# Optimization experiments

Measured on AMD Instinct MI355X. Metric: run time of the kernel, lower is better.

## Reference

```python
import jax, jax.numpy as jnp
import numpy as np

B, L, D, H = 4, 2048, 1024, 16
DH = D // H
SCALE = DH ** -0.5


def setup_inputs() -> dict:
    key = jax.random.key(0)
    ks = jax.random.split(key, 8)
    q = jax.random.normal(ks[0], (B, L, D), dtype=jnp.float32)
    k = jax.random.normal(ks[1], (B, L, D), dtype=jnp.float32)
    v = jax.random.normal(ks[2], (B, L, D), dtype=jnp.float32)
    mask = jax.random.randint(ks[3], (B, 1, L), 0, 2, dtype=jnp.int32)
    s = D ** -0.5
    Wq = jax.random.normal(ks[4], (D, D), dtype=jnp.float32) * s
    Wk = jax.random.normal(ks[5], (D, D), dtype=jnp.float32) * s
    Wv = jax.random.normal(ks[6], (D, D), dtype=jnp.float32) * s
    Wo = jax.random.normal(ks[7], (D, D), dtype=jnp.float32) * s
    return {"q": q, "k": k, "v": v, "mask": mask, "Wq": Wq, "Wk": Wk, "Wv": Wv, "Wo": Wo}


def reference(q, k, v, mask, Wq, Wk, Wv, Wo):
    b, l, d = q.shape
    # torch Linear (no bias): x @ W^T; split heads -> [B, H, T, DH]
    qh = (q @ Wq.T).reshape(b, l, H, DH).transpose(0, 2, 1, 3)
    kh = (k @ Wk.T).reshape(b, -1, H, DH).transpose(0, 2, 1, 3)
    vh = (v @ Wv.T).reshape(b, -1, H, DH).transpose(0, 2, 1, 3)
    # scores [B, H, L, S]
    scores = jnp.einsum('bhld,bhsd->bhls', qh, kh) * SCALE
    scores = jnp.where(mask[:, None, :, :] != 1, jnp.float32(-1e9), scores)
    attn = jax.nn.softmax(scores, axis=-1)  # dropout defined but never applied in original forward
    out = jnp.einsum('bhls,bhsd->bhld', attn, vh)
    out = out.transpose(0, 2, 1, 3).reshape(b, l, d)
    return out @ Wo.T
```

## Files before the change

### kernel.cpp

```cpp
#include <hip/hip_runtime.h>
#include <cstddef>
#include <cstdint>

#define BB 4
#define LL 2048
#define DD 1024
#define HH 16
#define DHD 64
#define QSCALE 0.18033688f

typedef short s16x8 __attribute__((ext_vector_type(8)));
typedef short s16x4 __attribute__((ext_vector_type(4)));
typedef float f32x4 __attribute__((ext_vector_type(4)));
typedef unsigned int u32;
typedef u32 u32x2 __attribute__((ext_vector_type(2)));

__device__ __forceinline__ short f2bf(float f) {
  union { float f; u32 u; } x; x.f = f;
  u32 r = x.u + 0x7FFFu + ((x.u >> 16) & 1u);
  return (short)(r >> 16);
}
__device__ __forceinline__ u32 pack2bf(float a, float b) {
  union { float f; u32 u; } x, y; x.f = a; y.f = b;
  return __builtin_amdgcn_perm(y.u + 0x8000u, x.u + 0x8000u, 0x07060302u);
}
__device__ __forceinline__ void gl2lds16(const short* g, short* l) {
  __builtin_amdgcn_global_load_lds(
      (const __attribute__((address_space(1))) unsigned int*)g,
      (__attribute__((address_space(3))) unsigned int*)l, 16, 0, 0);
}

__global__ __launch_bounds__(256) void cast_x_kernel(const float* __restrict__ q,
                                                     const float* __restrict__ k,
                                                     const float* __restrict__ v,
                                                     short* __restrict__ qb,
                                                     short* __restrict__ kb,
                                                     short* __restrict__ vb) {
  const float* s; short* d;
  if (blockIdx.y == 0) { s = q; d = qb; }
  else if (blockIdx.y == 1) { s = k; d = kb; }
  else { s = v; d = vb; }
  int i = blockIdx.x * 256 + threadIdx.x;
  float4 x = ((const float4*)s)[i];
  s16x4 o; o.x = f2bf(x.x); o.y = f2bf(x.y); o.z = f2bf(x.z); o.w = f2bf(x.w);
  ((s16x4*)d)[i] = o;
}

__global__ __launch_bounds__(256) void cast_w_kernel(const float* __restrict__ Wq,
                                                     const float* __restrict__ Wk,
                                                     const float* __restrict__ Wv,
                                                     const float* __restrict__ Wo,
                                                     short* __restrict__ Wqb,
                                                     short* __restrict__ Wkb,
                                                     short* __restrict__ Wvb,
                                                     short* __restrict__ Wob) {
  const float* s; short* d; float sc = 1.0f;
  if (blockIdx.y == 0) { s = Wq; d = Wqb; sc = QSCALE; }
  else if (blockIdx.y == 1) { s = Wk; d = Wkb; }
  else if (blockIdx.y == 2) { s = Wv; d = Wvb; }
  else { s = Wo; d = Wob; }
  int i = blockIdx.x * 256 + threadIdx.x;
  float4 x = ((const float4*)s)[i];
  s16x4 o; o.x = f2bf(x.x * sc); o.y = f2bf(x.y * sc); o.z = f2bf(x.z * sc); o.w = f2bf(x.w * sc);
  ((s16x4*)d)[i] = o;
}

__global__ __launch_bounds__(256) void mask_kernel(const int* __restrict__ mask,
                                                   float* __restrict__ maskadd) {
  int i = blockIdx.x * 256 + threadIdx.x;
  int4 m = ((const int4*)mask)[i];
  f32x4 o;
  o[0] = (m.x == 1) ? 0.0f : -30000.0f;
  o[1] = (m.y == 1) ? 0.0f : -30000.0f;
  o[2] = (m.z == 1) ? 0.0f : -30000.0f;
  o[3] = (m.w == 1) ? 0.0f : -30000.0f;
  ((f32x4*)maskadd)[i] = o;
}

__device__ __forceinline__ void gemm_core(const short* __restrict__ A, const short* __restrict__ B,
                                          int K, int bm, int bn, short* As, short* Bs,
                                          f32x4 (&acc)[4][4]) {
  const int tid = threadIdx.x;
  const int lane = tid & 63, wave = tid >> 6;
  const int wv = __builtin_amdgcn_readfirstlane(wave);
  const int quad = lane >> 4, l16 = lane & 15;
  const int wm = (wave >> 1) * 64, wn = (wave & 1) * 64;
  const short* ap[4]; const short* bp[4]; short* la[4]; short* lb[4];
#pragma unroll
  for (int t = 0; t < 4; ++t) {
    int s = wv * 256 + t * 64 + lane;
    int r = s >> 3, gl = (s & 7) ^ (r & 7);
    ap[t] = A + (size_t)(bm + r) * K + gl * 8;
    bp[t] = B + (size_t)(bn + r) * K + gl * 8;
    la[t] = &As[(wv * 256 + t * 64) * 8];
    lb[t] = &Bs[(wv * 256 + t * 64) * 8];
  }
  const int sw0 = (quad ^ (l16 & 7)) * 8;
  const int sw1 = ((4 + quad) ^ (l16 & 7)) * 8;
  for (int kk = 0; kk < K; kk += 64) {
    __syncthreads();
#pragma unroll
    for (int t = 0; t < 4; ++t) gl2lds16(ap[t] + kk, la[t]);
#pragma unroll
    for (int t = 0; t < 4; ++t) gl2lds16(bp[t] + kk, lb[t]);
    __syncthreads();
#pragma unroll
    for (int c = 0; c < 2; ++c) {
      const int sw = c ? sw1 : sw0;
      s16x8 af[4], bf[4];
#pragma unroll
      for (int t = 0; t < 4; ++t) af[t] = *(const s16x8*)&As[(wm + t * 16 + l16) * 64 + sw];
#pragma unroll
      for (int t = 0; t < 4; ++t) bf[t] = *(const s16x8*)&Bs[(wn + t * 16 + l16) * 64 + sw];
#pragma unroll
      for (int mt = 0; mt < 4; ++mt)
#pragma unroll
        for (int nt = 0; nt < 4; ++nt)
          acc[mt][nt] = __builtin_amdgcn_mfma_f32_16x16x32_bf16(af[mt], bf[nt], acc[mt][nt], 0, 0, 0);
    }
  }
}

__global__ __launch_bounds__(256) void qkv_gemm(const short* __restrict__ qb, const short* __restrict__ kb,
                                                const short* __restrict__ vb, const short* __restrict__ Wqb,
                                                const short* __restrict__ Wkb, const short* __restrict__ Wvb,
                                                short* __restrict__ Qh, short* __restrict__ Kh,
                                                short* __restrict__ VT) {
  __shared__ short As[128 * 64];
  __shared__ short Bs[128 * 64];
  const int z = blockIdx.z;
  const short *A, *B; short* C;
  if (z == 0) { A = qb; B = Wqb; C = Qh; }
  else if (z == 1) { A = kb; B = Wkb; C = Kh; }
  else { A = Wvb; B = vb; C = VT; }
  const int bm = (z == 2 ? blockIdx.x : (int)blockIdx.y) * 128;
  const int bn = (z == 2 ? (int)blockIdx.y : (int)blockIdx.x) * 128;
  f32x4 acc[4][4] = {};
  gemm_core(A, B, DD, bm, bn, As, Bs, acc);

  const int lane = threadIdx.x & 63, wave = threadIdx.x >> 6;
  const int quad = lane >> 4, l16 = lane & 15;
  const int wm = (wave >> 1) * 64, wn = (wave & 1) * 64;
#pragma unroll
  for (int mt = 0; mt < 4; ++mt)
#pragma unroll
    for (int nt = 0; nt < 4; ++nt)
#pragma unroll
      for (int i = 0; i < 4; ++i) {
        int m = bm + wm + mt * 16 + quad * 4 + i;
        int n = bn + wn + nt * 16 + l16;
        float val = acc[mt][nt][i];
        if (z < 2) {
          int b = m >> 11, l = m & 2047;
          C[((size_t)(b * HH + (n >> 6)) << 17) + (size_t)l * DHD + (n & 63)] = f2bf(val);
        } else {
          int b = n >> 11, l = n & 2047;
          C[((size_t)(b * DD + m) << 11) + l] = f2bf(val);
        }
      }
}

__global__ __launch_bounds__(256) void out_gemm(const short* __restrict__ A, const short* __restrict__ B,
                                                float* __restrict__ C) {
  __shared__ short As[128 * 64];
  __shared__ short Bs[128 * 64];
  const int bm = blockIdx.y * 128, bn = blockIdx.x * 128;
  f32x4 acc[4][4] = {};
  gemm_core(A, B, DD, bm, bn, As, Bs, acc);
  const int lane = threadIdx.x & 63, wave = threadIdx.x >> 6;
  const int quad = lane >> 4, l16 = lane & 15;
  const int wm = (wave >> 1) * 64, wn = (wave & 1) * 64;
#pragma unroll
  for (int mt = 0; mt < 4; ++mt)
#pragma unroll
    for (int nt = 0; nt < 4; ++nt)
#pragma unroll
      for (int i = 0; i < 4; ++i) {
        int m = bm + wm + mt * 16 + quad * 4 + i;
        int n = bn + wn + nt * 16 + l16;
        C[(size_t)m * DD + n] = acc[mt][nt][i];
      }
}

__global__ __launch_bounds__(256, 4) void attn_kernel(const short* __restrict__ Qh,
                                                      const short* __restrict__ Kh,
                                                      const short* __restrict__ VT,
                                                      const float* __restrict__ maskadd,
                                                      short* __restrict__ AO) {
  __shared__ short Ks[64 * 64];
  __shared__ short Vs[64 * 64];
  __shared__ short Pb[8 * 16 * 64];
  const int tid  = threadIdx.x;
  const int lane = tid & 63, wave = tid >> 6;
  const int wv   = __builtin_amdgcn_readfirstlane(wave);
  const int quad = lane >> 4, l16 = lane & 15;
  const int a7 = l16 & 7, q1 = quad >> 1, qlo = quad & 1;
  const int bh = blockIdx.y, b = bh >> 4;
  const int q0 = blockIdx.x * 128;

  const float* mrow = maskadd + b * LL;
  const short* Qb = Qh + (size_t)bh * LL * DHD;
  const short* Kb = Kh + (size_t)bh * LL * DHD;
  const short* Vb = VT + (size_t)bh * DHD * LL;

  s16x8 qf[2][2];
#pragma unroll
  for (int u = 0; u < 2; ++u)
#pragma unroll
    for (int c = 0; c < 2; ++c)
      qf[u][c] = *(const s16x8*)&Qb[(size_t)(q0 + wv * 32 + u * 16 + l16) * DHD + c * 32 + quad * 8];

  const short* kp[2]; const short* vp[2]; short* lk[2]; short* lv[2];
#pragma unroll
  for (int t = 0; t < 2; ++t) {
    int s = wv * 128 + t * 64 + lane;
    int r = s >> 3, gl = (s & 7) ^ (r & 7);
    kp[t] = Kb + (size_t)r * DHD + gl * 8;
    vp[t] = Vb + (size_t)r * LL + gl * 8;
    lk[t] = &Ks[(wv * 128 + t * 64) * 8];
    lv[t] = &Vs[(wv * 128 + t * 64) * 8];
  }
  const int sw0 = (quad ^ a7) * 8;
  const int sw1 = ((4 + quad) ^ a7) * 8;

  s16x8 vone;
#pragma unroll
  for (int j = 0; j < 8; ++j) vone[j] = (short)0x3F80;

  f32x4 lsum[2] = {};
  f32x4 accO[2][4] = {};
  short* pb = &Pb[wave * 2048 + l16 * 64 + qlo * 4];

  for (int s0 = 0; s0 < LL; s0 += 64) {
    f32x4 mm[4];
#pragma unroll
    for (int st = 0; st < 4; ++st) mm[st] = *(const f32x4*)&mrow[s0 + st * 16 + quad * 4];
    __syncthreads();
#pragma unroll
    for (int t = 0; t < 2; ++t) gl2lds16(kp[t] + (size_t)s0 * DHD, lk[t]);
#pragma unroll
    for (int t = 0; t < 2; ++t) gl2lds16(vp[t] + s0, lv[t]);
    __syncthreads();

    s16x8 kf[4][2];
#pragma unroll
    for (int st = 0; st < 4; ++st) {
      kf[st][0] = *(const s16x8*)&Ks[(st * 16 + l16) * 64 + sw0];
      kf[st][1] = *(const s16x8*)&Ks[(st * 16 + l16) * 64 + sw1];
    }
    f32x4 sc[2][4];
#pragma unroll
    for (int u = 0; u < 2; ++u)
#pragma unroll
      for (int st = 0; st < 4; ++st) {
        sc[u][st] = __builtin_amdgcn_mfma_f32_16x16x32_bf16(kf[st][0], qf[u][0], mm[st], 0, 0, 0);
        sc[u][st] = __builtin_amdgcn_mfma_f32_16x16x32_bf16(kf[st][1], qf[u][1], sc[u][st], 0, 0, 0);
      }

#pragma unroll
    for (int u = 0; u < 2; ++u)
#pragma unroll
      for (int st = 0; st < 4; ++st) {
        float p0 = __builtin_amdgcn_exp2f(sc[u][st][0]);
        float p1 = __builtin_amdgcn_exp2f(sc[u][st][1]);
        float p2 = __builtin_amdgcn_exp2f(sc[u][st][2]);
        float p3 = __builtin_amdgcn_exp2f(sc[u][st][3]);
        u32x2 w; w[0] = pack2bf(p0, p1); w[1] = pack2bf(p2, p3);
        *(u32x2*)(pb + u * 1024 + (((st * 2 + q1) ^ a7) << 3)) = w;
      }

    s16x8 pf[2][2];
#pragma unroll
    for (int u = 0; u < 2; ++u)
#pragma unroll
      for (int c = 0; c < 2; ++c)
        pf[u][c] = *(const s16x8*)&Pb[(wave * 2 + u) * 1024 + l16 * 64 + (((c * 4 + quad) ^ a7) << 3)];
#pragma unroll
    for (int u = 0; u < 2; ++u) {
      lsum[u] = __builtin_amdgcn_mfma_f32_16x16x32_bf16(pf[u][0], vone, lsum[u], 0, 0, 0);
      lsum[u] = __builtin_amdgcn_mfma_f32_16x16x32_bf16(pf[u][1], vone, lsum[u], 0, 0, 0);
    }
#pragma unroll
    for (int dt = 0; dt < 4; ++dt) {
      s16x8 vf0 = *(const s16x8*)&Vs[(dt * 16 + l16) * 64 + sw0];
      s16x8 vf1 = *(const s16x8*)&Vs[(dt * 16 + l16) * 64 + sw1];
#pragma unroll
      for (int u = 0; u < 2; ++u) {
        accO[u][dt] = __builtin_amdgcn_mfma_f32_16x16x32_bf16(pf[u][0], vf0, accO[u][dt], 0, 0, 0);
        accO[u][dt] = __builtin_amdgcn_mfma_f32_16x16x32_bf16(pf[u][1], vf1, accO[u][dt], 0, 0, 0);
      }
    }
  }

  short* AOb = AO + (size_t)b * LL * DD + (size_t)(bh & 15) * DHD;
#pragma unroll
  for (int u = 0; u < 2; ++u) {
    f32x4 rl;
#pragma unroll
    for (int i = 0; i < 4; ++i) rl[i] = __builtin_amdgcn_rcpf(lsum[u][i]);
#pragma unroll
    for (int dt = 0; dt < 4; ++dt)
#pragma unroll
      for (int i = 0; i < 4; ++i) {
        int qr = q0 + wv * 32 + u * 16 + quad * 4 + i;
        AOb[(size_t)qr * DD + dt * 16 + l16] = f2bf(accO[u][dt][i] * rl[i]);
      }
  }
}

extern "C" void kernel_launch(void* const* d_in, const int* in_sizes, int n_in,
                              void* d_out, int out_size, void* d_ws, size_t ws_size,
                              hipStream_t stream) {
  const float* q   = (const float*)d_in[0];
  const float* k   = (const float*)d_in[1];
  const float* v   = (const float*)d_in[2];
  const int*  mask = (const int*)d_in[3];
  const float* Wq  = (const float*)d_in[4];
  const float* Wk  = (const float*)d_in[5];
  const float* Wv  = (const float*)d_in[6];
  const float* Wo  = (const float*)d_in[7];

  const size_t SX = (size_t)BB * LL * DD;
  const size_t SW = (size_t)DD * DD;
  short* w = (short*)d_ws;
  short* qb  = w;        short* kb  = qb + SX;  short* vb  = kb + SX;
  short* Wqb = vb + SX;  short* Wkb = Wqb + SW; short* Wvb = Wkb + SW; short* Wob = Wvb + SW;
  short* Qh  = Wob + SW; short* Kh  = Qh + SX;  short* VT  = Kh + SX;
  float* maskadd = (float*)(VT + SX);
  short* AO = qb;

  cast_x_kernel<<<dim3((unsigned)(SX / 4 / 256), 3), 256, 0, stream>>>(q, k, v, qb, kb, vb);
  cast_w_kernel<<<dim3((unsigned)(SW / 4 / 256), 4), 256, 0, stream>>>(Wq, Wk, Wv, Wo, Wqb, Wkb, Wvb, Wob);
  mask_kernel<<<BB * LL / 4 / 256, 256, 0, stream>>>(mask, maskadd);

  qkv_gemm<<<dim3(8, 64, 3), 256, 0, stream>>>(qb, kb, vb, Wqb, Wkb, Wvb, Qh, Kh, VT);
  attn_kernel<<<dim3(LL / 128, BB * HH), 256, 0, stream>>>(Qh, Kh, VT, maskadd, AO);
  out_gemm<<<dim3(8, 64), 256, 0, stream>>>(AO, Wob, (float*)d_out);
}
```

Before: 336.2 us.

## Fuse prep kernels, swizzle block order, double-buffer attention K/V, add setprio

Merges the three cast/mask kernels into one launch, which removes launch overhead. It remaps block IDs in all GEMM and attention grids so that blocks running at the same time share operand tiles in L2. The attention loop double-buffers the K/V tiles in LDS so the next tile's global-to-LDS load overlaps current compute, replacing two barriers per iteration with one. It also raises wave priority around MFMA bursts, at the cost of doubling K/V LDS use, which may reduce occupancy.

```diff
diff --git a/kernel.cpp b/kernel.cpp
--- a/kernel.cpp
+++ b/kernel.cpp
@@ -30,51 +30,54 @@
       (__attribute__((address_space(3))) unsigned int*)l, 16, 0, 0);
 }
 
-__global__ __launch_bounds__(256) void cast_x_kernel(const float* __restrict__ q,
-                                                     const float* __restrict__ k,
-                                                     const float* __restrict__ v,
-                                                     short* __restrict__ qb,
-                                                     short* __restrict__ kb,
-                                                     short* __restrict__ vb) {
-  const float* s; short* d;
-  if (blockIdx.y == 0) { s = q; d = qb; }
-  else if (blockIdx.y == 1) { s = k; d = kb; }
-  else { s = v; d = vb; }
-  int i = blockIdx.x * 256 + threadIdx.x;
-  float4 x = ((const float4*)s)[i];
-  s16x4 o; o.x = f2bf(x.x); o.y = f2bf(x.y); o.z = f2bf(x.z); o.w = f2bf(x.w);
-  ((s16x4*)d)[i] = o;
-}
-
-__global__ __launch_bounds__(256) void cast_w_kernel(const float* __restrict__ Wq,
-                                                     const float* __restrict__ Wk,
-                                                     const float* __restrict__ Wv,
-                                                     const float* __restrict__ Wo,
-                                                     short* __restrict__ Wqb,
-                                                     short* __restrict__ Wkb,
-                                                     short* __restrict__ Wvb,
-                                                     short* __restrict__ Wob) {
-  const float* s; short* d; float sc = 1.0f;
-  if (blockIdx.y == 0) { s = Wq; d = Wqb; sc = QSCALE; }
-  else if (blockIdx.y == 1) { s = Wk; d = Wkb; }
-  else if (blockIdx.y == 2) { s = Wv; d = Wvb; }
-  else { s = Wo; d = Wob; }
-  int i = blockIdx.x * 256 + threadIdx.x;
-  float4 x = ((const float4*)s)[i];
-  s16x4 o; o.x = f2bf(x.x * sc); o.y = f2bf(x.y * sc); o.z = f2bf(x.z * sc); o.w = f2bf(x.w * sc);
-  ((s16x4*)d)[i] = o;
-}
-
-__global__ __launch_bounds__(256) void mask_kernel(const int* __restrict__ mask,
+__global__ __launch_bounds__(256) void prep_kernel(const float* __restrict__ q,
+                                                   const float* __restrict__ k,
+                                                   const float* __restrict__ v,
+                                                   const float* __restrict__ Wq,
+                                                   const float* __restrict__ Wk,
+                                                   const float* __restrict__ Wv,
+                                                   const float* __restrict__ Wo,
+                                                   const int* __restrict__ mask,
+                                                   short* __restrict__ qb,
+                                                   short* __restrict__ kb,
+                                                   short* __restrict__ vb,
+                                                   short* __restrict__ Wqb,
+                                                   short* __restrict__ Wkb,
+                                                   short* __restrict__ Wvb,
+                                                   short* __restrict__ Wob,
                                                    float* __restrict__ maskadd) {
-  int i = blockIdx.x * 256 + threadIdx.x;
-  int4 m = ((const int4*)mask)[i];
-  f32x4 o;
-  o[0] = (m.x == 1) ? 0.0f : -30000.0f;
-  o[1] = (m.y == 1) ? 0.0f : -30000.0f;
-  o[2] = (m.z == 1) ? 0.0f : -30000.0f;
-  o[3] = (m.w == 1) ? 0.0f : -30000.0f;
-  ((f32x4*)maskadd)[i] = o;
+  const int bb = blockIdx.x;
+  if (bb < 24576) {
+    const float* s; short* d;
+    const int y = bb >> 13;
+    if (y == 0) { s = q; d = qb; }
+    else if (y == 1) { s = k; d = kb; }
+    else { s = v; d = vb; }
+    int i = (bb & 8191) * 256 + threadIdx.x;
+    float4 x = ((const float4*)s)[i];
+    s16x4 o; o.x = f2bf(x.x); o.y = f2bf(x.y); o.z = f2bf(x.z); o.w = f2bf(x.w);
+    ((s16x4*)d)[i] = o;
+  } else if (bb < 28672) {
+    const int y = (bb - 24576) >> 10;
+    const float* s; short* d; float sc = 1.0f;
+    if (y == 0) { s = Wq; d = Wqb; sc = QSCALE; }
+    else if (y == 1) { s = Wk; d = Wkb; }
+    else if (y == 2) { s = Wv; d = Wvb; }
+    else { s = Wo; d = Wob; }
+    int i = ((bb - 24576) & 1023) * 256 + threadIdx.x;
+    float4 x = ((const float4*)s)[i];
+    s16x4 o; o.x = f2bf(x.x * sc); o.y = f2bf(x.y * sc); o.z = f2bf(x.z * sc); o.w = f2bf(x.w * sc);
+    ((s16x4*)d)[i] = o;
+  } else {
+    int i = (bb - 28672) * 256 + threadIdx.x;
+    int4 m = ((const int4*)mask)[i];
+    f32x4 o;
+    o[0] = (m.x == 1) ? 0.0f : -30000.0f;
+    o[1] = (m.y == 1) ? 0.0f : -30000.0f;
+    o[2] = (m.z == 1) ? 0.0f : -30000.0f;
+    o[3] = (m.w == 1) ? 0.0f : -30000.0f;
+    ((f32x4*)maskadd)[i] = o;
+  }
 }
 
 __device__ __forceinline__ void gemm_core(const short* __restrict__ A, const short* __restrict__ B,
@@ -112,11 +115,13 @@
       for (int t = 0; t < 4; ++t) af[t] = *(const s16x8*)&As[(wm + t * 16 + l16) * 64 + sw];
 #pragma unroll
       for (int t = 0; t < 4; ++t) bf[t] = *(const s16x8*)&Bs[(wn + t * 16 + l16) * 64 + sw];
+      __builtin_amdgcn_s_setprio(1);
 #pragma unroll
       for (int mt = 0; mt < 4; ++mt)
 #pragma unroll
         for (int nt = 0; nt < 4; ++nt)
           acc[mt][nt] = __builtin_amdgcn_mfma_f32_16x16x32_bf16(af[mt], bf[nt], acc[mt][nt], 0, 0, 0);
+      __builtin_amdgcn_s_setprio(0);
     }
   }
 }
@@ -128,13 +133,15 @@
                                                 short* __restrict__ VT) {
   __shared__ short As[128 * 64];
   __shared__ short Bs[128 * 64];
-  const int z = blockIdx.z;
+  const int bid = blockIdx.x + ((blockIdx.y + (blockIdx.z << 6)) << 3);
+  const int swz = (bid & 7) * 192 + (bid >> 3);
+  const int bx = swz & 7, by = (swz >> 3) & 63, z = swz >> 9;
   const short *A, *B; short* C;
   if (z == 0) { A = qb; B = Wqb; C = Qh; }
   else if (z == 1) { A = kb; B = Wkb; C = Kh; }
   else { A = Wvb; B = vb; C = VT; }
-  const int bm = (z == 2 ? blockIdx.x : (int)blockIdx.y) * 128;
-  const int bn = (z == 2 ? (int)blockIdx.y : (int)blockIdx.x) * 128;
+  const int bm = (z == 2 ? bx : by) * 128;
+  const int bn = (z == 2 ? by : bx) * 128;
   f32x4 acc[4][4] = {};
   gemm_core(A, B, DD, bm, bn, As, Bs, acc);
 
@@ -164,7 +171,10 @@
                                                 float* __restrict__ C) {
   __shared__ short As[128 * 64];
   __shared__ short Bs[128 * 64];
-  const int bm = blockIdx.y * 128, bn = blockIdx.x * 128;
+  const int bid = blockIdx.x + (blockIdx.y << 3);
+  const int swz = (bid & 7) * 64 + (bid >> 3);
+  const int bx = swz & 7, by = swz >> 3;
+  const int bm = by * 128, bn = bx * 128;
   f32x4 acc[4][4] = {};
   gemm_core(A, B, DD, bm, bn, As, Bs, acc);
   const int lane = threadIdx.x & 63, wave = threadIdx.x >> 6;
@@ -187,16 +197,20 @@
                                                       const short* __restrict__ VT,
                                                       const float* __restrict__ maskadd,
                                                       short* __restrict__ AO) {
-  __shared__ short Ks[64 * 64];
-  __shared__ short Vs[64 * 64];
+  __shared__ short Ks[2][64 * 64];
+  __shared__ short Vs[2][64 * 64];
   __shared__ short Pb[8 * 16 * 64];
   const int tid  = threadIdx.x;
   const int lane = tid & 63, wave = tid >> 6;
   const int wv   = __builtin_amdgcn_readfirstlane(wave);
   const int quad = lane >> 4, l16 = lane & 15;
   const int a7 = l16 & 7, q1 = quad >> 1, qlo = quad & 1;
-  const int bh = blockIdx.y, b = bh >> 4;
-  const int q0 = blockIdx.x * 128;
+
+  const int bid = blockIdx.x + (blockIdx.y << 4);
+  const int swz = (bid & 7) * 128 + (bid >> 3);
+  const int bx = swz & 15, bh = swz >> 4;
+  const int b = bh >> 4;
+  const int q0 = bx * 128;
 
   const float* mrow = maskadd + b * LL;
   const short* Qb = Qh + (size_t)bh * LL * DHD;
@@ -210,15 +224,14 @@
     for (int c = 0; c < 2; ++c)
       qf[u][c] = *(const s16x8*)&Qb[(size_t)(q0 + wv * 32 + u * 16 + l16) * DHD + c * 32 + quad * 8];
 
-  const short* kp[2]; const short* vp[2]; short* lk[2]; short* lv[2];
+  const short* kp[2]; const short* vp[2]; int off[2];
 #pragma unroll
   for (int t = 0; t < 2; ++t) {
     int s = wv * 128 + t * 64 + lane;
     int r = s >> 3, gl = (s & 7) ^ (r & 7);
     kp[t] = Kb + (size_t)r * DHD + gl * 8;
     vp[t] = Vb + (size_t)r * LL + gl * 8;
-    lk[t] = &Ks[(wv * 128 + t * 64) * 8];
-    lv[t] = &Vs[(wv * 128 + t * 64) * 8];
+    off[t] = (wv * 128 + t * 64) * 8;
   }
   const int sw0 = (quad ^ a7) * 8;
   const int sw1 = ((4 + quad) ^ a7) * 8;
@@ -231,24 +244,34 @@
   f32x4 accO[2][4] = {};
   short* pb = &Pb[wave * 2048 + l16 * 64 + qlo * 4];
 
+#pragma unroll
+  for (int t = 0; t < 2; ++t) gl2lds16(kp[t], &Ks[0][off[t]]);
+#pragma unroll
+  for (int t = 0; t < 2; ++t) gl2lds16(vp[t], &Vs[0][off[t]]);
+
+  int cur = 0;
   for (int s0 = 0; s0 < LL; s0 += 64) {
+    __syncthreads();
+    if (s0 + 64 < LL) {
+#pragma unroll
+      for (int t = 0; t < 2; ++t) gl2lds16(kp[t] + (size_t)(s0 + 64) * DHD, &Ks[cur ^ 1][off[t]]);
+#pragma unroll
+      for (int t = 0; t < 2; ++t) gl2lds16(vp[t] + (s0 + 64), &Vs[cur ^ 1][off[t]]);
+    }
     f32x4 mm[4];
 #pragma unroll
     for (int st = 0; st < 4; ++st) mm[st] = *(const f32x4*)&mrow[s0 + st * 16 + quad * 4];
-    __syncthreads();
-#pragma unroll
-    for (int t = 0; t < 2; ++t) gl2lds16(kp[t] + (size_t)s0 * DHD, lk[t]);
-#pragma unroll
-    for (int t = 0; t < 2; ++t) gl2lds16(vp[t] + s0, lv[t]);
-    __syncthreads();
-
+
+    const short* Kc = Ks[cur];
+    const short* Vc = Vs[cur];
     s16x8 kf[4][2];
 #pragma unroll
     for (int st = 0; st < 4; ++st) {
-      kf[st][0] = *(const s16x8*)&Ks[(st * 16 + l16) * 64 + sw0];
-      kf[st][1] = *(const s16x8*)&Ks[(st * 16 + l16) * 64 + sw1];
+      kf[st][0] = *(const s16x8*)&Kc[(st * 16 + l16) * 64 + sw0];
+      kf[st][1] = *(const s16x8*)&Kc[(st * 16 + l16) * 64 + sw1];
     }
     f32x4 sc[2][4];
+    __builtin_amdgcn_s_setprio(1);
 #pragma unroll
     for (int u = 0; u < 2; ++u)
 #pragma unroll
@@ -256,6 +279,7 @@
         sc[u][st] = __builtin_amdgcn_mfma_f32_16x16x32_bf16(kf[st][0], qf[u][0], mm[st], 0, 0, 0);
         sc[u][st] = __builtin_amdgcn_mfma_f32_16x16x32_bf16(kf[st][1], qf[u][1], sc[u][st], 0, 0, 0);
       }
+    __builtin_amdgcn_s_setprio(0);
 
 #pragma unroll
     for (int u = 0; u < 2; ++u)
@@ -275,6 +299,7 @@
 #pragma unroll
       for (int c = 0; c < 2; ++c)
         pf[u][c] = *(const s16x8*)&Pb[(wave * 2 + u) * 1024 + l16 * 64 + (((c * 4 + quad) ^ a7) << 3)];
+    __builtin_amdgcn_s_setprio(1);
 #pragma unroll
     for (int u = 0; u < 2; ++u) {
       lsum[u] = __builtin_amdgcn_mfma_f32_16x16x32_bf16(pf[u][0], vone, lsum[u], 0, 0, 0);
@@ -282,14 +307,16 @@
     }
 #pragma unroll
     for (int dt = 0; dt < 4; ++dt) {
-      s16x8 vf0 = *(const s16x8*)&Vs[(dt * 16 + l16) * 64 + sw0];
-      s16x8 vf1 = *(const s16x8*)&Vs[(dt * 16 + l16) * 64 + sw1];
+      s16x8 vf0 = *(const s16x8*)&Vc[(dt * 16 + l16) * 64 + sw0];
+      s16x8 vf1 = *(const s16x8*)&Vc[(dt * 16 + l16) * 64 + sw1];
 #pragma unroll
       for (int u = 0; u < 2; ++u) {
         accO[u][dt] = __builtin_amdgcn_mfma_f32_16x16x32_bf16(pf[u][0], vf0, accO[u][dt], 0, 0, 0);
         accO[u][dt] = __builtin_amdgcn_mfma_f32_16x16x32_bf16(pf[u][1], vf1, accO[u][dt], 0, 0, 0);
       }
     }
+    __builtin_amdgcn_s_setprio(0);
+    cur ^= 1;
   }
 
   short* AOb = AO + (size_t)b * LL * DD + (size_t)(bh & 15) * DHD;
@@ -329,10 +356,8 @@
   float* maskadd = (float*)(VT + SX);
   short* AO = qb;
 
-  cast_x_kernel<<<dim3((unsigned)(SX / 4 / 256), 3), 256, 0, stream>>>(q, k, v, qb, kb, vb);
-  cast_w_kernel<<<dim3((unsigned)(SW / 4 / 256), 4), 256, 0, stream>>>(Wq, Wk, Wv, Wo, Wqb, Wkb, Wvb, Wob);
-  mask_kernel<<<BB * LL / 4 / 256, 256, 0, stream>>>(mask, maskadd);
-
+  prep_kernel<<<28680, 256, 0, stream>>>(q, k, v, Wq, Wk, Wv, Wo, mask,
+                                         qb, kb, vb, Wqb, Wkb, Wvb, Wob, maskadd);
   qkv_gemm<<<dim3(8, 64, 3), 256, 0, stream>>>(qb, kb, vb, Wqb, Wkb, Wvb, Qh, Kh, VT);
   attn_kernel<<<dim3(LL / 128, BB * HH), 256, 0, stream>>>(Qh, Kh, VT, maskadd, AO);
   out_gemm<<<dim3(8, 64), 256, 0, stream>>>(AO, Wob, (float*)d_out);
```

Result: no change. 337.4 us (+0.4%).
